# Kernel tuning notes

Measured on AMD Instinct MI355X. Metric: run time of the kernel, lower is better.

The kernel has to match this reference:

```python
import jax, jax.numpy as jnp
import numpy as np

DIM = 1024
NUM_HEADS = 16
HEAD_DIM = DIM // NUM_HEADS
EPS = 1e-6


def layer_norm(x, gamma, beta):
    # normalize over last dim (head_dim)
    mu = jnp.mean(x, axis=-1, keepdims=True)
    var = jnp.mean(jnp.square(x - mu), axis=-1, keepdims=True)
    return (x - mu) / jnp.sqrt(var + EPS) * gamma + beta


def apply_rope(q, k):
    # q, k: [B, S, H, D]; computed in fp32 (attn_fp32=True)
    seq_len, head_dim = q.shape[1], q.shape[3]
    half = head_dim // 2
    freq_range = jnp.arange(half, dtype=jnp.float32) / half
    inv_freq = 1.0 / (10000.0 ** freq_range)                       # [half]
    t = jnp.arange(seq_len, dtype=jnp.float32)                     # [S]
    freqs = jnp.outer(t, inv_freq)                                 # [S, half]
    emb = jnp.concatenate([freqs, freqs], axis=-1)                 # [S, D]
    cos = jnp.cos(emb)[None, :, None, :]                           # [1, S, 1, D]
    sin = jnp.sin(emb)[None, :, None, :]

    def rotate_half(x):
        x1, x2 = x[..., :half], x[..., half:]
        return jnp.concatenate([-x2, x1], axis=-1)

    return q * cos + rotate_half(q) * sin, k * cos + rotate_half(k) * sin


def setup_inputs() -> dict:
    key = jax.random.key(0)
    ks = jax.random.split(key, 4)
    B, S = 2, 2048
    x = jax.random.normal(ks[0], (B, S, DIM), dtype=jnp.float32)
    # xavier-uniform-ish scale for linear weights (torch Linear layout: [out, in])
    lim_qkv = float(np.sqrt(6.0 / (DIM + 3 * DIM)))
    w_qkv = jax.random.uniform(ks[1], (3 * DIM, DIM), dtype=jnp.float32, minval=-lim_qkv, maxval=lim_qkv)
    lim_p = float(np.sqrt(6.0 / (DIM + DIM)))
    w_proj = jax.random.uniform(ks[2], (DIM, DIM), dtype=jnp.float32, minval=-lim_p, maxval=lim_p)
    b_proj = jnp.zeros((DIM,), dtype=jnp.float32)
    q_gamma = jnp.ones((HEAD_DIM,), dtype=jnp.float32)
    q_beta = jnp.zeros((HEAD_DIM,), dtype=jnp.float32)
    k_gamma = jnp.ones((HEAD_DIM,), dtype=jnp.float32)
    k_beta = jnp.zeros((HEAD_DIM,), dtype=jnp.float32)
    return {"x": x, "w_qkv": w_qkv, "w_proj": w_proj, "b_proj": b_proj,
            "q_gamma": q_gamma, "q_beta": q_beta, "k_gamma": k_gamma, "k_beta": k_beta}


def reference(x, w_qkv, w_proj, b_proj, q_gamma, q_beta, k_gamma, k_beta):
    B, S, C = x.shape
    H, D = NUM_HEADS, HEAD_DIM
    qkv = jnp.einsum('bsc,oc->bso', x, w_qkv).reshape(B, S, 3, H, D)
    q = layer_norm(qkv[:, :, 0], q_gamma, q_beta)   # [B, S, H, D]
    k = layer_norm(qkv[:, :, 1], k_gamma, k_beta)
    v = qkv[:, :, 2]
    q, k = apply_rope(q, k)
    # attn_fp32=True: scores in fp32
    scale = D ** (-0.5)
    q = q.astype(jnp.float32) * scale
    k = k.astype(jnp.float32)
    v = v.astype(jnp.float32)
    attn = jnp.einsum('bqhd,bkhd->bhqk', q, k)      # [B, H, S, S]
    attn = jax.nn.softmax(attn, axis=-1)
    out = jnp.einsum('bhqk,bkhd->bqhd', attn, v).reshape(B, S, C)
    out = jnp.einsum('bsc,oc->bso', out, w_proj) + b_proj
    return out
```

## Files before the change

kernel.cpp:

```cpp
#include <hip/hip_runtime.h>
#include <math.h>

#define DIM   1024
#define NH    16
#define HD    64
#define BATCH 2
#define SEQ   2048
#define EPS   1e-6f

#define NX  (BATCH * SEQ * DIM)
#define NWQ (3 * DIM * DIM)
#define NWP (DIM * DIM)
#define NCONVBLK ((NX + NWQ + NWP) / 8 / 256)
#define NTABBLK  (SEQ * 32 / 256)

typedef __attribute__((ext_vector_type(8))) short bf16x8;
typedef __attribute__((ext_vector_type(4))) float f32x4;

#define EXP2F(x) __builtin_amdgcn_exp2f(x)
#define LOG2E 1.4426950408889634f

__device__ __forceinline__ float bf2f(unsigned short u) {
  return __uint_as_float(((unsigned int)u) << 16);
}
__device__ __forceinline__ unsigned short f2bf(float f) {
  unsigned int u = __float_as_uint(f);
  unsigned int r = (u + 0x7FFFu + ((u >> 16) & 1u)) >> 16;
  return (unsigned short)r;
}
__device__ __forceinline__ unsigned int pack_bf16_trunc(float p0, float p1) {
  return __builtin_amdgcn_perm(__float_as_uint(p1), __float_as_uint(p0), 0x07060302u);
}

__device__ __forceinline__ void async_copy16(const void* g, void* l) {
  __builtin_amdgcn_global_load_lds(
      (const __attribute__((address_space(1))) unsigned int*)g,
      (__attribute__((address_space(3))) unsigned int*)l, 16, 0, 0);
}


__global__ __launch_bounds__(256)
void prep(const void* __restrict__ x, const void* __restrict__ wq,
          const void* __restrict__ wp,
          unsigned short* __restrict__ xb, unsigned short* __restrict__ wqb,
          unsigned short* __restrict__ wpb, float2* __restrict__ tab,
          int* __restrict__ flag) {
  const int bid = blockIdx.x, tid = threadIdx.x;

  if (bid >= NCONVBLK) {
    const int idx = (bid - NCONVBLK) * 256 + tid;
    const int s = idx >> 5, f = idx & 31;
    const float invf = expf(-((float)f * (1.f / 32.f)) * 9.210340371976184f);
    float sn, cs;
    sincosf((float)s * invf, &sn, &cs);
    tab[idx] = make_float2(cs, sn);
    return;
  }

  __shared__ int cnt;
  if (tid == 0) cnt = 0;
  __syncthreads();
  {
    unsigned short u = ((const unsigned short*)wq)[tid];
    if ((u & 0x7F80u) >= 0x3F80u) atomicAdd(&cnt, 1);
  }
  __syncthreads();
  const bool isf32 = (cnt >= 16);
  if (bid == 0 && tid == 0) *flag = isf32 ? 1 : 0;

  int i = (bid * 256 + tid) * 8;
  const void* src;
  unsigned short* dst;
  if (i < NX) { src = x; dst = xb; }
  else if (i < NX + NWQ) { src = wq; dst = wqb; i -= NX; }
  else { src = wp; dst = wpb; i -= NX + NWQ; }
  if (isf32) {
    const float* s = (const float*)src + i;
    float4 a = *(const float4*)s;
    float4 b = *(const float4*)(s + 4);
    ushort4 lo, hi;
    lo.x = f2bf(a.x); lo.y = f2bf(a.y); lo.z = f2bf(a.z); lo.w = f2bf(a.w);
    hi.x = f2bf(b.x); hi.y = f2bf(b.y); hi.z = f2bf(b.z); hi.w = f2bf(b.w);
    *(ushort4*)&dst[i] = lo;
    *(ushort4*)&dst[i + 4] = hi;
  } else {
    *(uint4*)&dst[i] = *(const uint4*)((const unsigned short*)src + i);
  }
}

__device__ __forceinline__ float ld_param(const void* p, bool isf32, int idx) {
  return isf32 ? ((const float*)p)[idx] : bf2f(((const unsigned short*)p)[idx]);
}

__global__ __launch_bounds__(512)
void gemm_qkv(const unsigned short* __restrict__ A, const unsigned short* __restrict__ B,
              unsigned short* __restrict__ Qb, unsigned short* __restrict__ Kb,
              unsigned short* __restrict__ VbT,
              const void* __restrict__ qg, const void* __restrict__ qbe,
              const void* __restrict__ kg, const void* __restrict__ kbe,
              const float2* __restrict__ tab, const int* __restrict__ flagp) {
  __shared__ __attribute__((aligned(16))) unsigned short As[2][128 * 32];
  __shared__ __attribute__((aligned(16))) unsigned short Bs[2][128 * 32];

  const int K = DIM;
  const int tid  = threadIdx.x;
  const int wv   = tid >> 6;
  const int lane = tid & 63;
  const int l15  = lane & 15;
  const int quad = lane >> 4;
  const int wm = wv & 3;
  const int wn = wv >> 2;
  const int bm = blockIdx.y * 128;
  const int bn = blockIdx.x * 128;
  const int qsw = (quad ^ ((l15 >> 1) & 3)) * 8;

  f32x4 acc[2][4];
#pragma unroll
  for (int i = 0; i < 2; ++i)
#pragma unroll
    for (int j = 0; j < 4; ++j) acc[i][j] = (f32x4){0.f, 0.f, 0.f, 0.f};

  const int srow = tid >> 2;
  const int kseg = (((tid & 3) ^ ((tid >> 3) & 3))) * 8;
  const unsigned short* Ag = A + (size_t)(bm + srow) * K + kseg;
  const unsigned short* Bg = B + (size_t)(bn + srow) * K + kseg;

  async_copy16(Ag, &As[0][wv * 512]);
  async_copy16(Bg, &Bs[0][wv * 512]);
  __syncthreads();

  for (int k0 = 0; k0 < K; k0 += 32) {
    const int cur = (k0 >> 5) & 1, nxt = cur ^ 1;
    if (k0 + 32 < K) {
      async_copy16(Ag + k0 + 32, &As[nxt][wv * 512]);
      async_copy16(Bg + k0 + 32, &Bs[nxt][wv * 512]);
    }

    bf16x8 af[2], bf[4];
#pragma unroll
    for (int mt = 0; mt < 2; ++mt)
      af[mt] = *(const bf16x8*)&As[cur][(wm * 32 + mt * 16 + l15) * 32 + qsw];
#pragma unroll
    for (int nt = 0; nt < 4; ++nt)
      bf[nt] = *(const bf16x8*)&Bs[cur][(wn * 64 + nt * 16 + l15) * 32 + qsw];
#pragma unroll
    for (int mt = 0; mt < 2; ++mt)
#pragma unroll
      for (int nt = 0; nt < 4; ++nt)
        acc[mt][nt] = __builtin_amdgcn_mfma_f32_16x16x32_bf16(af[mt], bf[nt], acc[mt][nt], 0, 0, 0);
    __syncthreads();
  }

  const bool isf32 = (*flagp != 0);
  const int type = bn >> 10;
  const int h = ((bn & 1023) >> 6) + wn;

  if (type == 2) {
#pragma unroll
    for (int mt = 0; mt < 2; ++mt) {
      const int r0 = bm + wm * 32 + mt * 16 + quad * 4;
      const int b = r0 >> 11, s0 = r0 & 2047;
#pragma unroll
      for (int nt = 0; nt < 4; ++nt) {
        const int d = nt * 16 + l15;
        uint2 pk;
        pk.x = ((unsigned int)f2bf(acc[mt][nt][1]) << 16) | f2bf(acc[mt][nt][0]);
        pk.y = ((unsigned int)f2bf(acc[mt][nt][3]) << 16) | f2bf(acc[mt][nt][2]);
        *(uint2*)&VbT[((size_t)(b * NH + h) * HD + d) * SEQ + s0] = pk;
      }
    }
    return;
  }

  unsigned short* plane = (type == 0) ? Qb : Kb;
  const void* gp = (type == 0) ? qg : kg;
  const void* bp = (type == 0) ? qbe : kbe;
  float gam[4], bet[4];
#pragma unroll
  for (int nt = 0; nt < 4; ++nt) {
    gam[nt] = ld_param(gp, isf32, nt * 16 + l15);
    bet[nt] = ld_param(bp, isf32, nt * 16 + l15);
  }
  const float scale = (type == 0) ? (0.125f * LOG2E) : 1.f;

#pragma unroll
  for (int mt = 0; mt < 2; ++mt)
#pragma unroll
    for (int rr = 0; rr < 4; ++rr) {
      const int r = bm + wm * 32 + mt * 16 + quad * 4 + rr;
      const int b = r >> 11, s = r & 2047;
      float sum = acc[mt][0][rr] + acc[mt][1][rr] + acc[mt][2][rr] + acc[mt][3][rr];
      sum += __shfl_xor(sum, 1); sum += __shfl_xor(sum, 2);
      sum += __shfl_xor(sum, 4); sum += __shfl_xor(sum, 8);
      const float mu = sum * (1.f / 64.f);
      float vs = 0.f;
#pragma unroll
      for (int nt = 0; nt < 4; ++nt) {
        const float d = acc[mt][nt][rr] - mu;
        vs += d * d;
      }
      vs += __shfl_xor(vs, 1); vs += __shfl_xor(vs, 2);
      vs += __shfl_xor(vs, 4); vs += __shfl_xor(vs, 8);
      const float rs = rsqrtf(vs * (1.f / 64.f) + EPS);
      float xn[4];
#pragma unroll
      for (int nt = 0; nt < 4; ++nt)
        xn[nt] = (acc[mt][nt][rr] - mu) * rs * gam[nt] + bet[nt];
      const float2 t0 = tab[s * 32 + l15];
      const float2 t1 = tab[s * 32 + 16 + l15];
      float ro[4];
      ro[0] = xn[0] * t0.x - xn[2] * t0.y;
      ro[2] = xn[2] * t0.x + xn[0] * t0.y;
      ro[1] = xn[1] * t1.x - xn[3] * t1.y;
      ro[3] = xn[3] * t1.x + xn[1] * t1.y;
      unsigned short* row = plane + (((size_t)(b * NH + h) * SEQ + s) * HD);
#pragma unroll
      for (int nt = 0; nt < 4; ++nt)
        row[nt * 16 + l15] = f2bf(ro[nt] * scale);
    }
}

#define KIDX(g,k0,key,dim) (((((g)*2+(k0))*64+(key))*32)+(dim))
#define VOFF 8192
#define POFF 16384
#define PIDX(w,row,col) (POFF + ((w)*32+(row))*72 + (col))

__global__ __launch_bounds__(512, 4)
void attn_mfma6(const unsigned short* __restrict__ Qb, const unsigned short* __restrict__ Kb,
                const unsigned short* __restrict__ VbT, unsigned short* __restrict__ O) {
  __shared__ __attribute__((aligned(16))) unsigned short SMEM[34816];

  const int tid  = threadIdx.x;
  const int wv   = tid >> 6;
  const int g    = wv >> 2;
  const int qsub = wv & 3;
  const int lane = tid & 63;
  const int l15  = lane & 15;
  const int quad = lane >> 4;
  const int bh = blockIdx.y;
  const int q0 = blockIdx.x * 128;
  const size_t base  = (size_t)bh * (SEQ * HD);
  const size_t baseT = (size_t)bh * (HD * SEQ);
  const int qsw = (quad ^ ((l15 >> 1) & 3)) * 8;

  bf16x8 qf[2][2];
#pragma unroll
  for (int mt = 0; mt < 2; ++mt)
#pragma unroll
    for (int k0 = 0; k0 < 2; ++k0)
      qf[mt][k0] = *(const bf16x8*)&Qb[base + (size_t)(q0 + qsub * 32 + mt * 16 + l15) * HD + k0 * 32 + quad * 8];

  bf16x8 ones;
#pragma unroll
  for (int j = 0; j < 8; ++j) ones[j] = (short)0x3F80;

  f32x4 oaccT[4][2];
  f32x4 ol[2];
#pragma unroll
  for (int nb = 0; nb < 4; ++nb)
#pragma unroll
    for (int mt = 0; mt < 2; ++mt) oaccT[nb][mt] = (f32x4){0.f, 0.f, 0.f, 0.f};
  ol[0] = (f32x4){0.f, 0.f, 0.f, 0.f};
  ol[1] = (f32x4){0.f, 0.f, 0.f, 0.f};

  const int sseg = (((lane & 3) ^ ((lane >> 3) & 3))) * 8;
  const unsigned short* srcK = Kb + base + (size_t)(qsub * 16 + (lane >> 2)) * HD + sseg;
  const unsigned short* srcV = VbT + baseT + (size_t)(qsub * 16 + (lane >> 2)) * SEQ + sseg;
  unsigned short* dstK0 = &SMEM[KIDX(g, 0, qsub * 16, 0)];
  unsigned short* dstK1 = &SMEM[KIDX(g, 1, qsub * 16, 0)];
  unsigned short* dstV0 = &SMEM[VOFF + KIDX(g, 0, qsub * 16, 0)];
  unsigned short* dstV1 = &SMEM[VOFF + KIDX(g, 1, qsub * 16, 0)];

  for (int it = 0; it < SEQ / 128; ++it) {
    const int kt = it * 128 + g * 64;
    __syncthreads();
    async_copy16(srcK + (size_t)kt * HD,      dstK0);
    async_copy16(srcK + (size_t)kt * HD + 32, dstK1);
    async_copy16(srcV + kt,                   dstV0);
    async_copy16(srcV + kt + 32,              dstV1);
    __syncthreads();

    f32x4 st[4][2];
#pragma unroll
    for (int nb = 0; nb < 4; ++nb)
#pragma unroll
      for (int mt = 0; mt < 2; ++mt) st[nb][mt] = (f32x4){0.f, 0.f, 0.f, 0.f};
#pragma unroll
    for (int k0 = 0; k0 < 2; ++k0)
#pragma unroll
      for (int nb = 0; nb < 4; ++nb) {
        bf16x8 kf = *(const bf16x8*)&SMEM[KIDX(g, k0, nb * 16 + l15, qsw)];
#pragma unroll
        for (int mt = 0; mt < 2; ++mt)
          st[nb][mt] = __builtin_amdgcn_mfma_f32_16x16x32_bf16(kf, qf[mt][k0], st[nb][mt], 0, 0, 0);
      }

#pragma unroll
    for (int mt = 0; mt < 2; ++mt)
#pragma unroll
      for (int nb = 0; nb < 4; ++nb) {
        const float p0 = EXP2F(st[nb][mt][0]);
        const float p1 = EXP2F(st[nb][mt][1]);
        const float p2 = EXP2F(st[nb][mt][2]);
        const float p3 = EXP2F(st[nb][mt][3]);
        uint2 pk;
        pk.x = pack_bf16_trunc(p0, p1);
        pk.y = pack_bf16_trunc(p2, p3);
        *(uint2*)&SMEM[PIDX(wv, mt * 16 + l15, nb * 16 + quad * 4)] = pk;
      }

#pragma unroll
    for (int k0 = 0; k0 < 2; ++k0) {
      bf16x8 pf0 = *(const bf16x8*)&SMEM[PIDX(wv, 0 * 16 + l15, k0 * 32 + quad * 8)];
      bf16x8 pf1 = *(const bf16x8*)&SMEM[PIDX(wv, 1 * 16 + l15, k0 * 32 + quad * 8)];
      ol[0] = __builtin_amdgcn_mfma_f32_16x16x32_bf16(ones, pf0, ol[0], 0, 0, 0);
      ol[1] = __builtin_amdgcn_mfma_f32_16x16x32_bf16(ones, pf1, ol[1], 0, 0, 0);
#pragma unroll
      for (int nb = 0; nb < 4; ++nb) {
        bf16x8 vf = *(const bf16x8*)&SMEM[VOFF + KIDX(g, k0, nb * 16 + l15, qsw)];
        oaccT[nb][0] = __builtin_amdgcn_mfma_f32_16x16x32_bf16(vf, pf0, oaccT[nb][0], 0, 0, 0);
        oaccT[nb][1] = __builtin_amdgcn_mfma_f32_16x16x32_bf16(vf, pf1, oaccT[nb][1], 0, 0, 0);
      }
    }
  }

  __syncthreads();
  f32x4* MO = (f32x4*)SMEM;
  float* ML = (float*)(SMEM + POFF);
  if (g == 1) {
#pragma unroll
    for (int mt = 0; mt < 2; ++mt) {
#pragma unroll
      for (int nb = 0; nb < 4; ++nb)
        MO[(((qsub * 2 + mt) * 4 + nb) << 6) + lane] = oaccT[nb][mt];
      if (quad == 0)
        ML[(qsub * 2 + mt) * 16 + l15] = ol[mt][0];
    }
  }
  __syncthreads();
  if (g == 0) {
    const int b = bh >> 4, h = bh & 15;
#pragma unroll
    for (int mt = 0; mt < 2; ++mt) {
      const float l1 = ML[(qsub * 2 + mt) * 16 + l15];
      const float inv = 1.f / (ol[mt][0] + l1);
      const int qrow = q0 + qsub * 32 + mt * 16 + l15;
      unsigned short* orow = O + ((size_t)(b * SEQ + qrow)) * DIM + h * HD;
#pragma unroll
      for (int nb = 0; nb < 4; ++nb) {
        f32x4 o1 = MO[(((qsub * 2 + mt) * 4 + nb) << 6) + lane];
        uint2 pk;
        pk.x = ((unsigned int)f2bf((oaccT[nb][mt][1] + o1[1]) * inv) << 16) |
               f2bf((oaccT[nb][mt][0] + o1[0]) * inv);
        pk.y = ((unsigned int)f2bf((oaccT[nb][mt][3] + o1[3]) * inv) << 16) |
               f2bf((oaccT[nb][mt][2] + o1[2]) * inv);
        *(uint2*)&orow[nb * 16 + quad * 4] = pk;
      }
    }
  }
}

__global__ __launch_bounds__(256)
void gemm_out(const unsigned short* __restrict__ A, const unsigned short* __restrict__ B,
              const void* __restrict__ biasv, void* __restrict__ Cv,
              int M, int N, int K, const int* __restrict__ flagp) {
  __shared__ __attribute__((aligned(16))) unsigned short As[2][64 * 32];
  __shared__ __attribute__((aligned(16))) unsigned short Bs[2][64 * 32];

  const int tid  = threadIdx.x;
  const int wv   = tid >> 6;
  const int lane = tid & 63;
  const int l15  = lane & 15;
  const int quad = lane >> 4;
  const int wm = wv & 1, wn = wv >> 1;
  const int bm = blockIdx.y * 64;
  const int bn = blockIdx.x * 64;
  const int qsw = (quad ^ ((l15 >> 1) & 3)) * 8;

  f32x4 acc[2][2];
#pragma unroll
  for (int i = 0; i < 2; ++i)
#pragma unroll
    for (int j = 0; j < 2; ++j) acc[i][j] = (f32x4){0.f, 0.f, 0.f, 0.f};

  const int srow = tid >> 2;
  const int kseg = (((tid & 3) ^ ((tid >> 3) & 3))) * 8;
  const unsigned short* Ag = A + (size_t)(bm + srow) * K + kseg;
  const unsigned short* Bg = B + (size_t)(bn + srow) * K + kseg;

  async_copy16(Ag, &As[0][wv * 512]);
  async_copy16(Bg, &Bs[0][wv * 512]);
  __syncthreads();

  for (int k0 = 0; k0 < K; k0 += 32) {
    const int cur = (k0 >> 5) & 1, nxt = cur ^ 1;
    if (k0 + 32 < K) {
      async_copy16(Ag + k0 + 32, &As[nxt][wv * 512]);
      async_copy16(Bg + k0 + 32, &Bs[nxt][wv * 512]);
    }

    bf16x8 af[2], bf[2];
#pragma unroll
    for (int mt = 0; mt < 2; ++mt)
      af[mt] = *(const bf16x8*)&As[cur][(wm * 32 + mt * 16 + l15) * 32 + qsw];
#pragma unroll
    for (int nt = 0; nt < 2; ++nt)
      bf[nt] = *(const bf16x8*)&Bs[cur][(wn * 32 + nt * 16 + l15) * 32 + qsw];
#pragma unroll
    for (int mt = 0; mt < 2; ++mt)
#pragma unroll
      for (int nt = 0; nt < 2; ++nt)
        acc[mt][nt] = __builtin_amdgcn_mfma_f32_16x16x32_bf16(af[mt], bf[nt], acc[mt][nt], 0, 0, 0);
    __syncthreads();
  }

  const bool isf32 = (*flagp != 0);
#pragma unroll
  for (int mt = 0; mt < 2; ++mt)
#pragma unroll
    for (int rr = 0; rr < 4; ++rr) {
      const int r = bm + wm * 32 + mt * 16 + quad * 4 + rr;
#pragma unroll
      for (int nt = 0; nt < 2; ++nt) {
        const int c = bn + wn * 32 + nt * 16 + l15;
        const float bias_c = isf32 ? ((const float*)biasv)[c]
                                   : bf2f(((const unsigned short*)biasv)[c]);
        const float o = acc[mt][nt][rr] + bias_c;
        if (isf32) ((float*)Cv)[(size_t)r * N + c] = o;
        else       ((unsigned short*)Cv)[(size_t)r * N + c] = f2bf(o);
      }
    }
}

extern "C" void kernel_launch(void* const* d_in, const int* in_sizes, int n_in,
                              void* d_out, int out_size, void* d_ws, size_t ws_size,
                              hipStream_t stream) {
  const void* x      = d_in[0];
  const void* w_qkv  = d_in[1];
  const void* w_proj = d_in[2];
  const void* b_proj = d_in[3];
  const void* q_g    = d_in[4];
  const void* q_b    = d_in[5];
  const void* k_g    = d_in[6];
  const void* k_b    = d_in[7];

  const size_t PLANE = (size_t)BATCH * NH * SEQ * HD;

  unsigned short* Qb  = (unsigned short*)d_ws;
  unsigned short* Kb  = Qb + PLANE;
  unsigned short* VbT = Kb + PLANE;
  unsigned short* xb  = VbT + PLANE;
  unsigned short* wqb = xb + PLANE;
  unsigned short* wpb = wqb + NWQ;
  float2* tab = (float2*)(wpb + NWP);
  int* flag = (int*)(tab + SEQ * 32);

  hipLaunchKernelGGL(prep, dim3(NCONVBLK + NTABBLK), dim3(256), 0, stream,
                     x, w_qkv, w_proj, xb, wqb, wpb, tab, flag);

  {
    dim3 grid((3 * DIM) / 128, (BATCH * SEQ) / 128);
    hipLaunchKernelGGL(gemm_qkv, grid, dim3(512), 0, stream,
                       xb, wqb, Qb, Kb, VbT, q_g, q_b, k_g, k_b, tab, flag);
  }
  {
    dim3 grid(SEQ / 128, BATCH * NH);
    hipLaunchKernelGGL(attn_mfma6, grid, dim3(512), 0, stream,
                       Qb, Kb, VbT, xb);
  }
  {
    dim3 grid(DIM / 64, (BATCH * SEQ) / 64);
    hipLaunchKernelGGL(gemm_out, grid, dim3(256), 0, stream,
                       xb, wpb, b_proj, d_out, BATCH * SEQ, DIM, DIM, flag);
  }
}
```

Baseline: 194.6 us.

## Fuse all four stages into one persistent kernel with grid barriers

Replaces the four separate launches (prep, QKV GEMM, attention, output GEMM) with one persistent kernel of 512 blocks that separates the stages with atomic grid-wide barriers. The block-level dtype-detection reduction becomes a per-wave ballot. The output GEMM is retiled to 64x128 with 8 waves. This aims to cut launch overhead and inter-kernel gaps, but it relies on all 512 blocks being co-resident for the spin barriers to work, and it adds a memset plus barrier spin cost. The QKV stage now runs 768 tiles over 512 blocks, which leaves some blocks idle for the second round.

```diff
diff --git a/kernel.cpp b/kernel.cpp
--- a/kernel.cpp
+++ b/kernel.cpp
@@ -11,8 +11,8 @@
 #define NX  (BATCH * SEQ * DIM)
 #define NWQ (3 * DIM * DIM)
 #define NWP (DIM * DIM)
-#define NCONVBLK ((NX + NWQ + NWP) / 8 / 256)
-#define NTABBLK  (SEQ * 32 / 256)
+#define NBLOCKS 512
+#define NTHREADS 512
 
 typedef __attribute__((ext_vector_type(8))) short bf16x8;
 typedef __attribute__((ext_vector_type(4))) float f32x4;
@@ -38,398 +38,381 @@
       (__attribute__((address_space(3))) unsigned int*)l, 16, 0, 0);
 }
 
-
-__global__ __launch_bounds__(256)
-void prep(const void* __restrict__ x, const void* __restrict__ wq,
-          const void* __restrict__ wp,
-          unsigned short* __restrict__ xb, unsigned short* __restrict__ wqb,
-          unsigned short* __restrict__ wpb, float2* __restrict__ tab,
-          int* __restrict__ flag) {
-  const int bid = blockIdx.x, tid = threadIdx.x;
-
-  if (bid >= NCONVBLK) {
-    const int idx = (bid - NCONVBLK) * 256 + tid;
-    const int s = idx >> 5, f = idx & 31;
-    const float invf = expf(-((float)f * (1.f / 32.f)) * 9.210340371976184f);
-    float sn, cs;
-    sincosf((float)s * invf, &sn, &cs);
-    tab[idx] = make_float2(cs, sn);
-    return;
-  }
-
-  __shared__ int cnt;
-  if (tid == 0) cnt = 0;
+__device__ __forceinline__ void grid_barrier(int* c) {
   __syncthreads();
-  {
-    unsigned short u = ((const unsigned short*)wq)[tid];
-    if ((u & 0x7F80u) >= 0x3F80u) atomicAdd(&cnt, 1);
+  if (threadIdx.x == 0) {
+    __hip_atomic_fetch_add(c, 1, __ATOMIC_ACQ_REL, __HIP_MEMORY_SCOPE_AGENT);
+    while (__hip_atomic_load(c, __ATOMIC_ACQUIRE, __HIP_MEMORY_SCOPE_AGENT) < NBLOCKS)
+      __builtin_amdgcn_s_sleep(2);
   }
   __syncthreads();
-  const bool isf32 = (cnt >= 16);
-  if (bid == 0 && tid == 0) *flag = isf32 ? 1 : 0;
-
-  int i = (bid * 256 + tid) * 8;
-  const void* src;
-  unsigned short* dst;
-  if (i < NX) { src = x; dst = xb; }
-  else if (i < NX + NWQ) { src = wq; dst = wqb; i -= NX; }
-  else { src = wp; dst = wpb; i -= NX + NWQ; }
-  if (isf32) {
-    const float* s = (const float*)src + i;
-    float4 a = *(const float4*)s;
-    float4 b = *(const float4*)(s + 4);
-    ushort4 lo, hi;
-    lo.x = f2bf(a.x); lo.y = f2bf(a.y); lo.z = f2bf(a.z); lo.w = f2bf(a.w);
-    hi.x = f2bf(b.x); hi.y = f2bf(b.y); hi.z = f2bf(b.z); hi.w = f2bf(b.w);
-    *(ushort4*)&dst[i] = lo;
-    *(ushort4*)&dst[i + 4] = hi;
-  } else {
-    *(uint4*)&dst[i] = *(const uint4*)((const unsigned short*)src + i);
-  }
 }
 
 __device__ __forceinline__ float ld_param(const void* p, bool isf32, int idx) {
   return isf32 ? ((const float*)p)[idx] : bf2f(((const unsigned short*)p)[idx]);
 }
 
-__global__ __launch_bounds__(512)
-void gemm_qkv(const unsigned short* __restrict__ A, const unsigned short* __restrict__ B,
-              unsigned short* __restrict__ Qb, unsigned short* __restrict__ Kb,
-              unsigned short* __restrict__ VbT,
-              const void* __restrict__ qg, const void* __restrict__ qbe,
-              const void* __restrict__ kg, const void* __restrict__ kbe,
-              const float2* __restrict__ tab, const int* __restrict__ flagp) {
-  __shared__ __attribute__((aligned(16))) unsigned short As[2][128 * 32];
-  __shared__ __attribute__((aligned(16))) unsigned short Bs[2][128 * 32];
-
-  const int K = DIM;
+
+#define KIDX(g,k0,key,dim) (((((g)*2+(k0))*64+(key))*32)+(dim))
+#define VOFF 8192
+#define POFF 16384
+#define PIDX(w,row,col) (POFF + ((w)*32+(row))*72 + (col))
+
+__global__ __launch_bounds__(512, 4)
+void fused(const void* __restrict__ x, const void* __restrict__ wq,
+           const void* __restrict__ wp, const void* __restrict__ bias,
+           const void* __restrict__ qg, const void* __restrict__ qbe,
+           const void* __restrict__ kg, const void* __restrict__ kbe,
+           unsigned short* __restrict__ Qb, unsigned short* __restrict__ Kb,
+           unsigned short* __restrict__ VbT, unsigned short* __restrict__ xb,
+           unsigned short* __restrict__ wqb, unsigned short* __restrict__ wpb,
+           float2* __restrict__ tab, int* __restrict__ sync,
+           void* __restrict__ out) {
+  __shared__ __attribute__((aligned(16))) unsigned short SMEM[34816];
+
+  const int bid  = blockIdx.x;
   const int tid  = threadIdx.x;
   const int wv   = tid >> 6;
   const int lane = tid & 63;
   const int l15  = lane & 15;
   const int quad = lane >> 4;
-  const int wm = wv & 3;
-  const int wn = wv >> 2;
-  const int bm = blockIdx.y * 128;
-  const int bn = blockIdx.x * 128;
-  const int qsw = (quad ^ ((l15 >> 1) & 3)) * 8;
-
-  f32x4 acc[2][4];
-#pragma unroll
-  for (int i = 0; i < 2; ++i)
-#pragma unroll
-    for (int j = 0; j < 4; ++j) acc[i][j] = (f32x4){0.f, 0.f, 0.f, 0.f};
-
-  const int srow = tid >> 2;
-  const int kseg = (((tid & 3) ^ ((tid >> 3) & 3))) * 8;
-  const unsigned short* Ag = A + (size_t)(bm + srow) * K + kseg;
-  const unsigned short* Bg = B + (size_t)(bn + srow) * K + kseg;
-
-  async_copy16(Ag, &As[0][wv * 512]);
-  async_copy16(Bg, &Bs[0][wv * 512]);
-  __syncthreads();
-
-  for (int k0 = 0; k0 < K; k0 += 32) {
-    const int cur = (k0 >> 5) & 1, nxt = cur ^ 1;
-    if (k0 + 32 < K) {
-      async_copy16(Ag + k0 + 32, &As[nxt][wv * 512]);
-      async_copy16(Bg + k0 + 32, &Bs[nxt][wv * 512]);
-    }
-
-    bf16x8 af[2], bf[4];
+  const int qsw  = (quad ^ ((l15 >> 1) & 3)) * 8;
+
+  bool isf32;
+  {
+    unsigned short u = ((const unsigned short*)wq)[lane];
+    unsigned long long m = __ballot((u & 0x7F80u) >= 0x3F80u);
+    isf32 = (__popcll(m) >= 8);
+  }
+
+  {
+    const int gtid = bid * NTHREADS + tid;
+    if (gtid < SEQ * 32) {
+      const int s = gtid >> 5, f = gtid & 31;
+      const float invf = expf(-((float)f * (1.f / 32.f)) * 9.210340371976184f);
+      float sn, cs;
+      sincosf((float)s * invf, &sn, &cs);
+      tab[gtid] = make_float2(cs, sn);
+    }
+    const int NG = (NX + NWQ + NWP) / 8;
+    for (int g8 = gtid; g8 < NG; g8 += NBLOCKS * NTHREADS) {
+      int i = g8 * 8;
+      const void* src;
+      unsigned short* dst;
+      if (i < NX) { src = x; dst = xb; }
+      else if (i < NX + NWQ) { src = wq; dst = wqb; i -= NX; }
+      else { src = wp; dst = wpb; i -= NX + NWQ; }
+      if (isf32) {
+        const float* s = (const float*)src + i;
+        float4 a = *(const float4*)s;
+        float4 b = *(const float4*)(s + 4);
+        ushort4 lo, hi;
+        lo.x = f2bf(a.x); lo.y = f2bf(a.y); lo.z = f2bf(a.z); lo.w = f2bf(a.w);
+        hi.x = f2bf(b.x); hi.y = f2bf(b.y); hi.z = f2bf(b.z); hi.w = f2bf(b.w);
+        *(ushort4*)&dst[i] = lo;
+        *(ushort4*)&dst[i + 4] = hi;
+      } else {
+        *(uint4*)&dst[i] = *(const uint4*)((const unsigned short*)src + i);
+      }
+    }
+  }
+  grid_barrier(&sync[0]);
+
+  for (int t = bid; t < 768; t += NBLOCKS) {
+    const int bm = (t / 24) * 128;
+    const int bn = (t % 24) * 128;
+    const int wm = wv & 3;
+    const int wn = wv >> 2;
+    unsigned short* As = SMEM;
+    unsigned short* Bs = SMEM + 8192;
+
+    f32x4 acc[2][4];
+#pragma unroll
+    for (int i = 0; i < 2; ++i)
+#pragma unroll
+      for (int j = 0; j < 4; ++j) acc[i][j] = (f32x4){0.f, 0.f, 0.f, 0.f};
+
+    const int srow = tid >> 2;
+    const int kseg = (((tid & 3) ^ ((tid >> 3) & 3))) * 8;
+    const unsigned short* Ag = xb + (size_t)(bm + srow) * DIM + kseg;
+    const unsigned short* Bg = wqb + (size_t)(bn + srow) * DIM + kseg;
+
+    async_copy16(Ag, &As[wv * 512]);
+    async_copy16(Bg, &Bs[wv * 512]);
+    __syncthreads();
+
+    for (int k0 = 0; k0 < DIM; k0 += 32) {
+      const int cur = (k0 >> 5) & 1, nxt = cur ^ 1;
+      if (k0 + 32 < DIM) {
+        async_copy16(Ag + k0 + 32, &As[nxt * 4096 + wv * 512]);
+        async_copy16(Bg + k0 + 32, &Bs[nxt * 4096 + wv * 512]);
+      }
+      bf16x8 af[2], bf[4];
+#pragma unroll
+      for (int mt = 0; mt < 2; ++mt)
+        af[mt] = *(const bf16x8*)&As[cur * 4096 + (wm * 32 + mt * 16 + l15) * 32 + qsw];
+#pragma unroll
+      for (int nt = 0; nt < 4; ++nt)
+        bf[nt] = *(const bf16x8*)&Bs[cur * 4096 + (wn * 64 + nt * 16 + l15) * 32 + qsw];
+#pragma unroll
+      for (int mt = 0; mt < 2; ++mt)
+#pragma unroll
+        for (int nt = 0; nt < 4; ++nt)
+          acc[mt][nt] = __builtin_amdgcn_mfma_f32_16x16x32_bf16(af[mt], bf[nt], acc[mt][nt], 0, 0, 0);
+      __syncthreads();
+    }
+
+    const int type = bn >> 10;
+    const int h = ((bn & 1023) >> 6) + wn;
+
+    if (type == 2) {
+#pragma unroll
+      for (int mt = 0; mt < 2; ++mt) {
+        const int r0 = bm + wm * 32 + mt * 16 + quad * 4;
+        const int b = r0 >> 11, s0 = r0 & 2047;
+#pragma unroll
+        for (int nt = 0; nt < 4; ++nt) {
+          const int d = nt * 16 + l15;
+          uint2 pk;
+          pk.x = ((unsigned int)f2bf(acc[mt][nt][1]) << 16) | f2bf(acc[mt][nt][0]);
+          pk.y = ((unsigned int)f2bf(acc[mt][nt][3]) << 16) | f2bf(acc[mt][nt][2]);
+          *(uint2*)&VbT[((size_t)(b * NH + h) * HD + d) * SEQ + s0] = pk;
+        }
+      }
+    } else {
+      unsigned short* plane = (type == 0) ? Qb : Kb;
+      const void* gp = (type == 0) ? qg : kg;
+      const void* bp = (type == 0) ? qbe : kbe;
+      float gam[4], bet[4];
+#pragma unroll
+      for (int nt = 0; nt < 4; ++nt) {
+        gam[nt] = ld_param(gp, isf32, nt * 16 + l15);
+        bet[nt] = ld_param(bp, isf32, nt * 16 + l15);
+      }
+      const float scale = (type == 0) ? (0.125f * LOG2E) : 1.f;
+#pragma unroll
+      for (int mt = 0; mt < 2; ++mt)
+#pragma unroll
+        for (int rr = 0; rr < 4; ++rr) {
+          const int r = bm + wm * 32 + mt * 16 + quad * 4 + rr;
+          const int b = r >> 11, s = r & 2047;
+          float sum = acc[mt][0][rr] + acc[mt][1][rr] + acc[mt][2][rr] + acc[mt][3][rr];
+          sum += __shfl_xor(sum, 1); sum += __shfl_xor(sum, 2);
+          sum += __shfl_xor(sum, 4); sum += __shfl_xor(sum, 8);
+          const float mu = sum * (1.f / 64.f);
+          float vs = 0.f;
+#pragma unroll
+          for (int nt = 0; nt < 4; ++nt) {
+            const float d = acc[mt][nt][rr] - mu;
+            vs += d * d;
+          }
+          vs += __shfl_xor(vs, 1); vs += __shfl_xor(vs, 2);
+          vs += __shfl_xor(vs, 4); vs += __shfl_xor(vs, 8);
+          const float rs = rsqrtf(vs * (1.f / 64.f) + EPS);
+          float xn[4];
+#pragma unroll
+          for (int nt = 0; nt < 4; ++nt)
+            xn[nt] = (acc[mt][nt][rr] - mu) * rs * gam[nt] + bet[nt];
+          const float2 t0 = tab[s * 32 + l15];
+          const float2 t1 = tab[s * 32 + 16 + l15];
+          float ro[4];
+          ro[0] = xn[0] * t0.x - xn[2] * t0.y;
+          ro[2] = xn[2] * t0.x + xn[0] * t0.y;
+          ro[1] = xn[1] * t1.x - xn[3] * t1.y;
+          ro[3] = xn[3] * t1.x + xn[1] * t1.y;
+          unsigned short* row = plane + (((size_t)(b * NH + h) * SEQ + s) * HD);
+#pragma unroll
+          for (int nt = 0; nt < 4; ++nt)
+            row[nt * 16 + l15] = f2bf(ro[nt] * scale);
+        }
+    }
+    __syncthreads();
+  }
+  grid_barrier(&sync[1]);
+
+  {
+    const int g    = wv >> 2;
+    const int qsub = wv & 3;
+    const int bh = bid >> 4;
+    const int q0 = (bid & 15) * 128;
+    const size_t base  = (size_t)bh * (SEQ * HD);
+    const size_t baseT = (size_t)bh * (HD * SEQ);
+
+    bf16x8 qf[2][2];
 #pragma unroll
     for (int mt = 0; mt < 2; ++mt)
-      af[mt] = *(const bf16x8*)&As[cur][(wm * 32 + mt * 16 + l15) * 32 + qsw];
-#pragma unroll
-    for (int nt = 0; nt < 4; ++nt)
-      bf[nt] = *(const bf16x8*)&Bs[cur][(wn * 64 + nt * 16 + l15) * 32 + qsw];
+#pragma unroll
+      for (int k0 = 0; k0 < 2; ++k0)
+        qf[mt][k0] = *(const bf16x8*)&Qb[base + (size_t)(q0 + qsub * 32 + mt * 16 + l15) * HD + k0 * 32 + quad * 8];
+
+    bf16x8 ones;
+#pragma unroll
+    for (int j = 0; j < 8; ++j) ones[j] = (short)0x3F80;
+
+    f32x4 oaccT[4][2];
+    f32x4 ol[2];
+#pragma unroll
+    for (int nb = 0; nb < 4; ++nb)
+#pragma unroll
+      for (int mt = 0; mt < 2; ++mt) oaccT[nb][mt] = (f32x4){0.f, 0.f, 0.f, 0.f};
+    ol[0] = (f32x4){0.f, 0.f, 0.f, 0.f};
+    ol[1] = (f32x4){0.f, 0.f, 0.f, 0.f};
+
+    const int sseg = (((lane & 3) ^ ((lane >> 3) & 3))) * 8;
+    const unsigned short* srcK = Kb + base + (size_t)(qsub * 16 + (lane >> 2)) * HD + sseg;
+    const unsigned short* srcV = VbT + baseT + (size_t)(qsub * 16 + (lane >> 2)) * SEQ + sseg;
+    unsigned short* dstK0 = &SMEM[KIDX(g, 0, qsub * 16, 0)];
+    unsigned short* dstK1 = &SMEM[KIDX(g, 1, qsub * 16, 0)];
+    unsigned short* dstV0 = &SMEM[VOFF + KIDX(g, 0, qsub * 16, 0)];
+    unsigned short* dstV1 = &SMEM[VOFF + KIDX(g, 1, qsub * 16, 0)];
+
+    for (int it = 0; it < SEQ / 128; ++it) {
+      const int kt = it * 128 + g * 64;
+      __syncthreads();
+      async_copy16(srcK + (size_t)kt * HD,      dstK0);
+      async_copy16(srcK + (size_t)kt * HD + 32, dstK1);
+      async_copy16(srcV + kt,                   dstV0);
+      async_copy16(srcV + kt + 32,              dstV1);
+      __syncthreads();
+
+      f32x4 st[4][2];
+#pragma unroll
+      for (int nb = 0; nb < 4; ++nb)
+#pragma unroll
+        for (int mt = 0; mt < 2; ++mt) st[nb][mt] = (f32x4){0.f, 0.f, 0.f, 0.f};
+#pragma unroll
+      for (int k0 = 0; k0 < 2; ++k0)
+#pragma unroll
+        for (int nb = 0; nb < 4; ++nb) {
+          bf16x8 kf = *(const bf16x8*)&SMEM[KIDX(g, k0, nb * 16 + l15, qsw)];
+#pragma unroll
+          for (int mt = 0; mt < 2; ++mt)
+            st[nb][mt] = __builtin_amdgcn_mfma_f32_16x16x32_bf16(kf, qf[mt][k0], st[nb][mt], 0, 0, 0);
+        }
+
+#pragma unroll
+      for (int mt = 0; mt < 2; ++mt)
+#pragma unroll
+        for (int nb = 0; nb < 4; ++nb) {
+          const float p0 = EXP2F(st[nb][mt][0]);
+          const float p1 = EXP2F(st[nb][mt][1]);
+          const float p2 = EXP2F(st[nb][mt][2]);
+          const float p3 = EXP2F(st[nb][mt][3]);
+          uint2 pk;
+          pk.x = pack_bf16_trunc(p0, p1);
+          pk.y = pack_bf16_trunc(p2, p3);
+          *(uint2*)&SMEM[PIDX(wv, mt * 16 + l15, nb * 16 + quad * 4)] = pk;
+        }
+
+#pragma unroll
+      for (int k0 = 0; k0 < 2; ++k0) {
+        bf16x8 pf0 = *(const bf16x8*)&SMEM[PIDX(wv, 0 * 16 + l15, k0 * 32 + quad * 8)];
+        bf16x8 pf1 = *(const bf16x8*)&SMEM[PIDX(wv, 1 * 16 + l15, k0 * 32 + quad * 8)];
+        ol[0] = __builtin_amdgcn_mfma_f32_16x16x32_bf16(ones, pf0, ol[0], 0, 0, 0);
+        ol[1] = __builtin_amdgcn_mfma_f32_16x16x32_bf16(ones, pf1, ol[1], 0, 0, 0);
+#pragma unroll
+        for (int nb = 0; nb < 4; ++nb) {
+          bf16x8 vf = *(const bf16x8*)&SMEM[VOFF + KIDX(g, k0, nb * 16 + l15, qsw)];
+          oaccT[nb][0] = __builtin_amdgcn_mfma_f32_16x16x32_bf16(vf, pf0, oaccT[nb][0], 0, 0, 0);
+          oaccT[nb][1] = __builtin_amdgcn_mfma_f32_16x16x32_bf16(vf, pf1, oaccT[nb][1], 0, 0, 0);
+        }
+      }
+    }
+
+    __syncthreads();
+    f32x4* MO = (f32x4*)SMEM;
+    float* ML = (float*)(SMEM + POFF);
+    if (g == 1) {
+#pragma unroll
+      for (int mt = 0; mt < 2; ++mt) {
+#pragma unroll
+        for (int nb = 0; nb < 4; ++nb)
+          MO[(((qsub * 2 + mt) * 4 + nb) << 6) + lane] = oaccT[nb][mt];
+        if (quad == 0)
+          ML[(qsub * 2 + mt) * 16 + l15] = ol[mt][0];
+      }
+    }
+    __syncthreads();
+    if (g == 0) {
+      const int b = bh >> 4, h = bh & 15;
+#pragma unroll
+      for (int mt = 0; mt < 2; ++mt) {
+        const float l1 = ML[(qsub * 2 + mt) * 16 + l15];
+        const float inv = 1.f / (ol[mt][0] + l1);
+        const int qrow = q0 + qsub * 32 + mt * 16 + l15;
+        unsigned short* orow = xb + ((size_t)(b * SEQ + qrow)) * DIM + h * HD;
+#pragma unroll
+        for (int nb = 0; nb < 4; ++nb) {
+          f32x4 o1 = MO[(((qsub * 2 + mt) * 4 + nb) << 6) + lane];
+          uint2 pk;
+          pk.x = ((unsigned int)f2bf((oaccT[nb][mt][1] + o1[1]) * inv) << 16) |
+                 f2bf((oaccT[nb][mt][0] + o1[0]) * inv);
+          pk.y = ((unsigned int)f2bf((oaccT[nb][mt][3] + o1[3]) * inv) << 16) |
+                 f2bf((oaccT[nb][mt][2] + o1[2]) * inv);
+          *(uint2*)&orow[nb * 16 + quad * 4] = pk;
+        }
+      }
+    }
+  }
+  grid_barrier(&sync[2]);
+
+  {
+    const int bm = (bid >> 3) * 64;
+    const int bn = (bid & 7) * 128;
+    const int wm = wv & 1, wn = wv >> 1;
+    unsigned short* Ao = SMEM;
+    unsigned short* Bo = SMEM + 4096;
+
+    f32x4 acc[2][2];
+#pragma unroll
+    for (int i = 0; i < 2; ++i)
+#pragma unroll
+      for (int j = 0; j < 2; ++j) acc[i][j] = (f32x4){0.f, 0.f, 0.f, 0.f};
+
+    const int kseg = (((lane & 3) ^ ((lane >> 3) & 3))) * 8;
+    const unsigned short* Ag = xb + (size_t)(bm + wv * 16 + (lane >> 2)) * DIM + kseg;
+    const unsigned short* Bg = wpb + (size_t)(bn + wv * 16 + (lane >> 2)) * DIM + kseg;
+
+    if (wv < 4) async_copy16(Ag, &Ao[wv * 512]);
+    async_copy16(Bg, &Bo[wv * 512]);
+    __syncthreads();
+
+    for (int k0 = 0; k0 < DIM; k0 += 32) {
+      const int cur = (k0 >> 5) & 1, nxt = cur ^ 1;
+      if (k0 + 32 < DIM) {
+        if (wv < 4) async_copy16(Ag + k0 + 32, &Ao[nxt * 2048 + wv * 512]);
+        async_copy16(Bg + k0 + 32, &Bo[nxt * 4096 + wv * 512]);
+      }
+      bf16x8 af[2], bf[2];
+#pragma unroll
+      for (int mt = 0; mt < 2; ++mt)
+        af[mt] = *(const bf16x8*)&Ao[cur * 2048 + (wm * 32 + mt * 16 + l15) * 32 + qsw];
+#pragma unroll
+      for (int nt = 0; nt < 2; ++nt)
+        bf[nt] = *(const bf16x8*)&Bo[cur * 4096 + (wn * 32 + nt * 16 + l15) * 32 + qsw];
+#pragma unroll
+      for (int mt = 0; mt < 2; ++mt)
+#pragma unroll
+        for (int nt = 0; nt < 2; ++nt)
+          acc[mt][nt] = __builtin_amdgcn_mfma_f32_16x16x32_bf16(af[mt], bf[nt], acc[mt][nt], 0, 0, 0);
+      __syncthreads();
+    }
+
 #pragma unroll
     for (int mt = 0; mt < 2; ++mt)
 #pragma unroll
-      for (int nt = 0; nt < 4; ++nt)
-        acc[mt][nt] = __builtin_amdgcn_mfma_f32_16x16x32_bf16(af[mt], bf[nt], acc[mt][nt], 0, 0, 0);
-    __syncthreads();
-  }
-
-  const bool isf32 = (*flagp != 0);
-  const int type = bn >> 10;
-  const int h = ((bn & 1023) >> 6) + wn;
-
-  if (type == 2) {
-#pragma unroll
-    for (int mt = 0; mt < 2; ++mt) {
-      const int r0 = bm + wm * 32 + mt * 16 + quad * 4;
-      const int b = r0 >> 11, s0 = r0 & 2047;
-#pragma unroll
-      for (int nt = 0; nt < 4; ++nt) {
-        const int d = nt * 16 + l15;
-        uint2 pk;
-        pk.x = ((unsigned int)f2bf(acc[mt][nt][1]) << 16) | f2bf(acc[mt][nt][0]);
-        pk.y = ((unsigned int)f2bf(acc[mt][nt][3]) << 16) | f2bf(acc[mt][nt][2]);
-        *(uint2*)&VbT[((size_t)(b * NH + h) * HD + d) * SEQ + s0] = pk;
-      }
-    }
-    return;
-  }
-
-  unsigned short* plane = (type == 0) ? Qb : Kb;
-  const void* gp = (type == 0) ? qg : kg;
-  const void* bp = (type == 0) ? qbe : kbe;
-  float gam[4], bet[4];
-#pragma unroll
-  for (int nt = 0; nt < 4; ++nt) {
-    gam[nt] = ld_param(gp, isf32, nt * 16 + l15);
-    bet[nt] = ld_param(bp, isf32, nt * 16 + l15);
-  }
-  const float scale = (type == 0) ? (0.125f * LOG2E) : 1.f;
-
-#pragma unroll
-  for (int mt = 0; mt < 2; ++mt)
-#pragma unroll
-    for (int rr = 0; rr < 4; ++rr) {
-      const int r = bm + wm * 32 + mt * 16 + quad * 4 + rr;
-      const int b = r >> 11, s = r & 2047;
-      float sum = acc[mt][0][rr] + acc[mt][1][rr] + acc[mt][2][rr] + acc[mt][3][rr];
-      sum += __shfl_xor(sum, 1); sum += __shfl_xor(sum, 2);
-      sum += __shfl_xor(sum, 4); sum += __shfl_xor(sum, 8);
-      const float mu = sum * (1.f / 64.f);
-      float vs = 0.f;
-#pragma unroll
-      for (int nt = 0; nt < 4; ++nt) {
-        const float d = acc[mt][nt][rr] - mu;
-        vs += d * d;
-      }
-      vs += __shfl_xor(vs, 1); vs += __shfl_xor(vs, 2);
-      vs += __shfl_xor(vs, 4); vs += __shfl_xor(vs, 8);
-      const float rs = rsqrtf(vs * (1.f / 64.f) + EPS);
-      float xn[4];
-#pragma unroll
-      for (int nt = 0; nt < 4; ++nt)
-        xn[nt] = (acc[mt][nt][rr] - mu) * rs * gam[nt] + bet[nt];
-      const float2 t0 = tab[s * 32 + l15];
-      const float2 t1 = tab[s * 32 + 16 + l15];
-      float ro[4];
-      ro[0] = xn[0] * t0.x - xn[2] * t0.y;
-      ro[2] = xn[2] * t0.x + xn[0] * t0.y;
-      ro[1] = xn[1] * t1.x - xn[3] * t1.y;
-      ro[3] = xn[3] * t1.x + xn[1] * t1.y;
-      unsigned short* row = plane + (((size_t)(b * NH + h) * SEQ + s) * HD);
-#pragma unroll
-      for (int nt = 0; nt < 4; ++nt)
-        row[nt * 16 + l15] = f2bf(ro[nt] * scale);
-    }
-}
-
-#define KIDX(g,k0,key,dim) (((((g)*2+(k0))*64+(key))*32)+(dim))
-#define VOFF 8192
-#define POFF 16384
-#define PIDX(w,row,col) (POFF + ((w)*32+(row))*72 + (col))
-
-__global__ __launch_bounds__(512, 4)
-void attn_mfma6(const unsigned short* __restrict__ Qb, const unsigned short* __restrict__ Kb,
-                const unsigned short* __restrict__ VbT, unsigned short* __restrict__ O) {
-  __shared__ __attribute__((aligned(16))) unsigned short SMEM[34816];
-
-  const int tid  = threadIdx.x;
-  const int wv   = tid >> 6;
-  const int g    = wv >> 2;
-  const int qsub = wv & 3;
-  const int lane = tid & 63;
-  const int l15  = lane & 15;
-  const int quad = lane >> 4;
-  const int bh = blockIdx.y;
-  const int q0 = blockIdx.x * 128;
-  const size_t base  = (size_t)bh * (SEQ * HD);
-  const size_t baseT = (size_t)bh * (HD * SEQ);
-  const int qsw = (quad ^ ((l15 >> 1) & 3)) * 8;
-
-  bf16x8 qf[2][2];
-#pragma unroll
-  for (int mt = 0; mt < 2; ++mt)
-#pragma unroll
-    for (int k0 = 0; k0 < 2; ++k0)
-      qf[mt][k0] = *(const bf16x8*)&Qb[base + (size_t)(q0 + qsub * 32 + mt * 16 + l15) * HD + k0 * 32 + quad * 8];
-
-  bf16x8 ones;
-#pragma unroll
-  for (int j = 0; j < 8; ++j) ones[j] = (short)0x3F80;
-
-  f32x4 oaccT[4][2];
-  f32x4 ol[2];
-#pragma unroll
-  for (int nb = 0; nb < 4; ++nb)
-#pragma unroll
-    for (int mt = 0; mt < 2; ++mt) oaccT[nb][mt] = (f32x4){0.f, 0.f, 0.f, 0.f};
-  ol[0] = (f32x4){0.f, 0.f, 0.f, 0.f};
-  ol[1] = (f32x4){0.f, 0.f, 0.f, 0.f};
-
-  const int sseg = (((lane & 3) ^ ((lane >> 3) & 3))) * 8;
-  const unsigned short* srcK = Kb + base + (size_t)(qsub * 16 + (lane >> 2)) * HD + sseg;
-  const unsigned short* srcV = VbT + baseT + (size_t)(qsub * 16 + (lane >> 2)) * SEQ + sseg;
-  unsigned short* dstK0 = &SMEM[KIDX(g, 0, qsub * 16, 0)];
-  unsigned short* dstK1 = &SMEM[KIDX(g, 1, qsub * 16, 0)];
-  unsigned short* dstV0 = &SMEM[VOFF + KIDX(g, 0, qsub * 16, 0)];
-  unsigned short* dstV1 = &SMEM[VOFF + KIDX(g, 1, qsub * 16, 0)];
-
-  for (int it = 0; it < SEQ / 128; ++it) {
-    const int kt = it * 128 + g * 64;
-    __syncthreads();
-    async_copy16(srcK + (size_t)kt * HD,      dstK0);
-    async_copy16(srcK + (size_t)kt * HD + 32, dstK1);
-    async_copy16(srcV + kt,                   dstV0);
-    async_copy16(srcV + kt + 32,              dstV1);
-    __syncthreads();
-
-    f32x4 st[4][2];
-#pragma unroll
-    for (int nb = 0; nb < 4; ++nb)
-#pragma unroll
-      for (int mt = 0; mt < 2; ++mt) st[nb][mt] = (f32x4){0.f, 0.f, 0.f, 0.f};
-#pragma unroll
-    for (int k0 = 0; k0 < 2; ++k0)
-#pragma unroll
-      for (int nb = 0; nb < 4; ++nb) {
-        bf16x8 kf = *(const bf16x8*)&SMEM[KIDX(g, k0, nb * 16 + l15, qsw)];
-#pragma unroll
-        for (int mt = 0; mt < 2; ++mt)
-          st[nb][mt] = __builtin_amdgcn_mfma_f32_16x16x32_bf16(kf, qf[mt][k0], st[nb][mt], 0, 0, 0);
-      }
-
-#pragma unroll
-    for (int mt = 0; mt < 2; ++mt)
-#pragma unroll
-      for (int nb = 0; nb < 4; ++nb) {
-        const float p0 = EXP2F(st[nb][mt][0]);
-        const float p1 = EXP2F(st[nb][mt][1]);
-        const float p2 = EXP2F(st[nb][mt][2]);
-        const float p3 = EXP2F(st[nb][mt][3]);
-        uint2 pk;
-        pk.x = pack_bf16_trunc(p0, p1);
-        pk.y = pack_bf16_trunc(p2, p3);
-        *(uint2*)&SMEM[PIDX(wv, mt * 16 + l15, nb * 16 + quad * 4)] = pk;
-      }
-
-#pragma unroll
-    for (int k0 = 0; k0 < 2; ++k0) {
-      bf16x8 pf0 = *(const bf16x8*)&SMEM[PIDX(wv, 0 * 16 + l15, k0 * 32 + quad * 8)];
-      bf16x8 pf1 = *(const bf16x8*)&SMEM[PIDX(wv, 1 * 16 + l15, k0 * 32 + quad * 8)];
-      ol[0] = __builtin_amdgcn_mfma_f32_16x16x32_bf16(ones, pf0, ol[0], 0, 0, 0);
-      ol[1] = __builtin_amdgcn_mfma_f32_16x16x32_bf16(ones, pf1, ol[1], 0, 0, 0);
-#pragma unroll
-      for (int nb = 0; nb < 4; ++nb) {
-        bf16x8 vf = *(const bf16x8*)&SMEM[VOFF + KIDX(g, k0, nb * 16 + l15, qsw)];
-        oaccT[nb][0] = __builtin_amdgcn_mfma_f32_16x16x32_bf16(vf, pf0, oaccT[nb][0], 0, 0, 0);
-        oaccT[nb][1] = __builtin_amdgcn_mfma_f32_16x16x32_bf16(vf, pf1, oaccT[nb][1], 0, 0, 0);
-      }
-    }
-  }
-
-  __syncthreads();
-  f32x4* MO = (f32x4*)SMEM;
-  float* ML = (float*)(SMEM + POFF);
-  if (g == 1) {
-#pragma unroll
-    for (int mt = 0; mt < 2; ++mt) {
-#pragma unroll
-      for (int nb = 0; nb < 4; ++nb)
-        MO[(((qsub * 2 + mt) * 4 + nb) << 6) + lane] = oaccT[nb][mt];
-      if (quad == 0)
-        ML[(qsub * 2 + mt) * 16 + l15] = ol[mt][0];
-    }
-  }
-  __syncthreads();
-  if (g == 0) {
-    const int b = bh >> 4, h = bh & 15;
-#pragma unroll
-    for (int mt = 0; mt < 2; ++mt) {
-      const float l1 = ML[(qsub * 2 + mt) * 16 + l15];
-      const float inv = 1.f / (ol[mt][0] + l1);
-      const int qrow = q0 + qsub * 32 + mt * 16 + l15;
-      unsigned short* orow = O + ((size_t)(b * SEQ + qrow)) * DIM + h * HD;
-#pragma unroll
-      for (int nb = 0; nb < 4; ++nb) {
-        f32x4 o1 = MO[(((qsub * 2 + mt) * 4 + nb) << 6) + lane];
-        uint2 pk;
-        pk.x = ((unsigned int)f2bf((oaccT[nb][mt][1] + o1[1]) * inv) << 16) |
-               f2bf((oaccT[nb][mt][0] + o1[0]) * inv);
-        pk.y = ((unsigned int)f2bf((oaccT[nb][mt][3] + o1[3]) * inv) << 16) |
-               f2bf((oaccT[nb][mt][2] + o1[2]) * inv);
-        *(uint2*)&orow[nb * 16 + quad * 4] = pk;
-      }
-    }
-  }
-}
-
-__global__ __launch_bounds__(256)
-void gemm_out(const unsigned short* __restrict__ A, const unsigned short* __restrict__ B,
-              const void* __restrict__ biasv, void* __restrict__ Cv,
-              int M, int N, int K, const int* __restrict__ flagp) {
-  __shared__ __attribute__((aligned(16))) unsigned short As[2][64 * 32];
-  __shared__ __attribute__((aligned(16))) unsigned short Bs[2][64 * 32];
-
-  const int tid  = threadIdx.x;
-  const int wv   = tid >> 6;
-  const int lane = tid & 63;
-  const int l15  = lane & 15;
-  const int quad = lane >> 4;
-  const int wm = wv & 1, wn = wv >> 1;
-  const int bm = blockIdx.y * 64;
-  const int bn = blockIdx.x * 64;
-  const int qsw = (quad ^ ((l15 >> 1) & 3)) * 8;
-
-  f32x4 acc[2][2];
-#pragma unroll
-  for (int i = 0; i < 2; ++i)
-#pragma unroll
-    for (int j = 0; j < 2; ++j) acc[i][j] = (f32x4){0.f, 0.f, 0.f, 0.f};
-
-  const int srow = tid >> 2;
-  const int kseg = (((tid & 3) ^ ((tid >> 3) & 3))) * 8;
-  const unsigned short* Ag = A + (size_t)(bm + srow) * K + kseg;
-  const unsigned short* Bg = B + (size_t)(bn + srow) * K + kseg;
-
-  async_copy16(Ag, &As[0][wv * 512]);
-  async_copy16(Bg, &Bs[0][wv * 512]);
-  __syncthreads();
-
-  for (int k0 = 0; k0 < K; k0 += 32) {
-    const int cur = (k0 >> 5) & 1, nxt = cur ^ 1;
-    if (k0 + 32 < K) {
-      async_copy16(Ag + k0 + 32, &As[nxt][wv * 512]);
-      async_copy16(Bg + k0 + 32, &Bs[nxt][wv * 512]);
-    }
-
-    bf16x8 af[2], bf[2];
-#pragma unroll
-    for (int mt = 0; mt < 2; ++mt)
-      af[mt] = *(const bf16x8*)&As[cur][(wm * 32 + mt * 16 + l15) * 32 + qsw];
-#pragma unroll
-    for (int nt = 0; nt < 2; ++nt)
-      bf[nt] = *(const bf16x8*)&Bs[cur][(wn * 32 + nt * 16 + l15) * 32 + qsw];
-#pragma unroll
-    for (int mt = 0; mt < 2; ++mt)
-#pragma unroll
-      for (int nt = 0; nt < 2; ++nt)
-        acc[mt][nt] = __builtin_amdgcn_mfma_f32_16x16x32_bf16(af[mt], bf[nt], acc[mt][nt], 0, 0, 0);
-    __syncthreads();
-  }
-
-  const bool isf32 = (*flagp != 0);
-#pragma unroll
-  for (int mt = 0; mt < 2; ++mt)
-#pragma unroll
-    for (int rr = 0; rr < 4; ++rr) {
-      const int r = bm + wm * 32 + mt * 16 + quad * 4 + rr;
-#pragma unroll
-      for (int nt = 0; nt < 2; ++nt) {
-        const int c = bn + wn * 32 + nt * 16 + l15;
-        const float bias_c = isf32 ? ((const float*)biasv)[c]
-                                   : bf2f(((const unsigned short*)biasv)[c]);
-        const float o = acc[mt][nt][rr] + bias_c;
-        if (isf32) ((float*)Cv)[(size_t)r * N + c] = o;
-        else       ((unsigned short*)Cv)[(size_t)r * N + c] = f2bf(o);
-      }
-    }
+      for (int rr = 0; rr < 4; ++rr) {
+        const int r = bm + wm * 32 + mt * 16 + quad * 4 + rr;
+#pragma unroll
+        for (int nt = 0; nt < 2; ++nt) {
+          const int c = bn + wn * 32 + nt * 16 + l15;
+          const float bias_c = ld_param(bias, isf32, c);
+          const float o = acc[mt][nt][rr] + bias_c;
+          if (isf32) ((float*)out)[(size_t)r * DIM + c] = o;
+          else       ((unsigned short*)out)[(size_t)r * DIM + c] = f2bf(o);
+        }
+      }
+  }
 }
 
 extern "C" void kernel_launch(void* const* d_in, const int* in_sizes, int n_in,
@@ -453,24 +436,10 @@
   unsigned short* wqb = xb + PLANE;
   unsigned short* wpb = wqb + NWQ;
   float2* tab = (float2*)(wpb + NWP);
-  int* flag = (int*)(tab + SEQ * 32);
-
-  hipLaunchKernelGGL(prep, dim3(NCONVBLK + NTABBLK), dim3(256), 0, stream,
-                     x, w_qkv, w_proj, xb, wqb, wpb, tab, flag);
-
-  {
-    dim3 grid((3 * DIM) / 128, (BATCH * SEQ) / 128);
-    hipLaunchKernelGGL(gemm_qkv, grid, dim3(512), 0, stream,
-                       xb, wqb, Qb, Kb, VbT, q_g, q_b, k_g, k_b, tab, flag);
-  }
-  {
-    dim3 grid(SEQ / 128, BATCH * NH);
-    hipLaunchKernelGGL(attn_mfma6, grid, dim3(512), 0, stream,
-                       Qb, Kb, VbT, xb);
-  }
-  {
-    dim3 grid(DIM / 64, (BATCH * SEQ) / 64);
-    hipLaunchKernelGGL(gemm_out, grid, dim3(256), 0, stream,
-                       xb, wpb, b_proj, d_out, BATCH * SEQ, DIM, DIM, flag);
-  }
-}
+  int* sync = (int*)(tab + SEQ * 32);
+
+  hipMemsetAsync(sync, 0, 4 * sizeof(int), stream);
+  hipLaunchKernelGGL(fused, dim3(NBLOCKS), dim3(NTHREADS), 0, stream,
+                     x, w_qkv, w_proj, b_proj, q_g, q_b, k_g, k_b,
+                     Qb, Kb, VbT, xb, wqb, wpb, tab, sync, d_out);
+}
```

Result: slower. 462.0 us (+137.4%).
